# Kernel tuning notes

Measured on AMD Instinct MI355X. Metric: run time of the kernel, lower is better.

Reference implementation:

```python
import jax, jax.numpy as jnp
import numpy as np

N_NODES = 100000
N_EDGES = 1600000
C_IN = 128
C_OUT = 128
BN_EPS = 1e-5


def setup_inputs() -> dict:
    key = jax.random.key(0)
    k = jax.random.split(key, 4)
    x = jax.random.normal(k[0], (N_NODES, C_IN), dtype=jnp.float32)
    edge_index = jax.random.randint(k[1], (2, N_EDGES), 0, N_NODES, dtype=jnp.int32)
    # nn.Linear params (Kaiming-uniform-ish scale)
    lim = 1.0 / np.sqrt(C_IN)
    W = jax.random.uniform(k[2], (C_IN, C_OUT), jnp.float32, -lim, lim)
    b = jnp.zeros((C_OUT,), jnp.float32)
    # BatchNorm (eval mode: running stats)
    gamma = jnp.ones((C_OUT,), jnp.float32)
    beta = jnp.zeros((C_OUT,), jnp.float32)
    running_mean = jnp.zeros((C_OUT,), jnp.float32)
    running_var = jnp.ones((C_OUT,), jnp.float32)
    return {"x": x, "edge_index": edge_index, "W": W, "b": b,
            "gamma": gamma, "beta": beta,
            "running_mean": running_mean, "running_var": running_var}


def reference(x, edge_index, W, b, gamma, beta, running_mean, running_var):
    # Linear projection: [N, C_in] @ [C_in, C_out]
    h = x @ W + b
    in_node, out_node = edge_index[0], edge_index[1]
    # gather edge features then scatter-mean onto destination nodes
    sums = jax.ops.segment_sum(h[in_node], out_node, num_segments=N_NODES)
    cnt = jax.ops.segment_sum(jnp.ones((in_node.shape[0],), h.dtype), out_node,
                              num_segments=N_NODES)
    agg = sums / jnp.maximum(cnt, 1.0)[:, None]  # mean; 0 for isolated nodes
    # BatchNorm1d (eval mode: running stats) + ReLU; dropout is identity in eval
    inv = jax.lax.rsqrt(running_var + BN_EPS)
    out = (agg - running_mean) * (inv * gamma) + beta
    return jax.nn.relu(out)
```

## Files before the change

kernel.cpp:

```cpp
#include <hip/hip_runtime.h>


#define NN 100000
#define NE 1600000
#define CC 128
#define BN_EPS 1e-5f
#define LBLK 1563
#define LSTR 136
#define NBUK 256
#define DPB 391
#define ACH 4096
#define ABLK 391
#define CAP 12288
#define GNB 64
#define CAP2 1536
#define BHS 16

typedef __attribute__((ext_vector_type(8))) short bf16x8;
typedef __attribute__((ext_vector_type(4))) float f32x4;

static __device__ __forceinline__ short f2bf(float f) {
  union { float f; unsigned u; } v; v.f = f;
  unsigned r = (v.u + 0x7FFF + ((v.u >> 16) & 1)) >> 16;
  return (short)r;
}
static __device__ __forceinline__ float bflo(unsigned p) {
  return __uint_as_float(p << 16);
}
static __device__ __forceinline__ float bfhi(unsigned p) {
  return __uint_as_float(p & 0xffff0000u);
}

static __device__ __forceinline__ int excl_scan256(int* a, int t, int v) {
  a[t] = v;
  __syncthreads();
  for (int d = 1; d < 256; d <<= 1) {
    const int x = (t >= d) ? a[t - d] : 0;
    __syncthreads();
    a[t] += x;
    __syncthreads();
  }
  const int incl = a[t];
  __syncthreads();
  a[t] = incl - v;
  __syncthreads();
  return incl - v;
}

__global__ __launch_bounds__(256) void prep_hist(
    const float* __restrict__ W, const float* __restrict__ bias,
    const float* __restrict__ gamma, const float* __restrict__ beta,
    const float* __restrict__ rmean, const float* __restrict__ rvar,
    const int* __restrict__ ei, short* __restrict__ Wsw,
    float* __restrict__ scsh, int* __restrict__ bhist) {
  __shared__ int lh[NBUK];
  const int t = threadIdx.x;
  const int i = blockIdx.x * 256 + t;
  if (i < CC * CC) {
    const int k = i >> 7, n = i & 127;
    const int nt = n & 7, m = n >> 3;
    const int kb = k >> 5, q = (k >> 3) & 3, j = k & 7;
    Wsw[(size_t)(((nt * 4 + kb) * 64 + (m + 16 * q)) * 8 + j)] = f2bf(W[i]);
  }
  if (i < CC) {
    const float sc = gamma[i] * rsqrtf(rvar[i] + BN_EPS);
    scsh[i] = sc;
    scsh[CC + i] = beta[i] - rmean[i] * sc;
    scsh[2 * CC + i] = bias[i];
  }
  lh[t] = 0;
  __syncthreads();
  const int e0 = blockIdx.x * ACH;
  const int e1 = min(NE, e0 + ACH);
  for (int e = e0 + t; e < e1; e += 256) atomicAdd(&lh[ei[NE + e] / DPB], 1);
  __syncthreads();
  if (lh[t]) atomicAdd(&bhist[t * BHS], lh[t]);
}

__global__ __launch_bounds__(256) void scatter_linear(
    const int* __restrict__ ei, const int* __restrict__ bhist,
    int* __restrict__ gcurz, int* __restrict__ ebuf,
    const float* __restrict__ x, const short* __restrict__ Wsw,
    const float* __restrict__ scsh, short* __restrict__ hout,
    int scat) {
  __shared__ __align__(16) char smem[50176];
  const int t = threadIdx.x;

  if (blockIdx.x < scat) {
    int2* sorted = (int2*)smem;
    int*  gsc    = (int*)(smem + 32768);
    int*  lh     = (int*)(smem + 33792);
    int*  lex    = (int*)(smem + 34816);
    int*  rb     = (int*)(smem + 35840);
    int*  lc     = (int*)(smem + 36864);
    const int e0 = blockIdx.x * ACH;
    const int e1 = min(NE, e0 + ACH);
    const int gbase = excl_scan256(gsc, t, bhist[t * BHS]);
    lh[t] = 0;
    __syncthreads();
    for (int e = e0 + t; e < e1; e += 256) atomicAdd(&lh[ei[NE + e] / DPB], 1);
    __syncthreads();
    const int vh = lh[t];
    const int lbase = excl_scan256(lex, t, vh);
    lc[t] = lbase;
    if (vh > 0) rb[t] = gbase + atomicAdd(&gcurz[t * BHS], vh);
    __syncthreads();
    for (int e = e0 + t; e < e1; e += 256) {
      const int src = ei[e], dst = ei[NE + e];
      const int p = atomicAdd(&lc[dst / DPB], 1);
      sorted[p] = make_int2(src, dst);
    }
    __syncthreads();
    const int n = e1 - e0;
    for (int i = t; i < n; i += 256) {
      const int2 v = sorted[i];
      const int b = v.y / DPB;
      ebuf[rb[b] + (i - lex[b])] = (v.x << 9) | (v.y - b * DPB);
    }
    return;
  }

  short* lsA = (short*)smem;
  short* lsW = (short*)(smem + 17408);
  const int n0 = (blockIdx.x - scat) * 64;

#pragma unroll
  for (int j = 0; j < 8; ++j) {
    const int idx = j * 256 + t;
    const int row = idx >> 5, kc4 = idx & 31;
    float4 v = make_float4(0.f, 0.f, 0.f, 0.f);
    if (n0 + row < NN) v = *(const float4*)(x + (size_t)(n0 + row) * CC + kc4 * 4);
    short4 sv;
    sv.x = f2bf(v.x); sv.y = f2bf(v.y); sv.z = f2bf(v.z); sv.w = f2bf(v.w);
    *(short4*)(lsA + row * LSTR + kc4 * 4) = sv;
  }
#pragma unroll
  for (int j = 0; j < 8; ++j) {
    const int idx = j * 256 + t;
    *(bf16x8*)(lsW + (size_t)idx * 8) = *(const bf16x8*)(Wsw + (size_t)idx * 8);
  }
  __syncthreads();

  const int wave = t >> 6, lane = t & 63;
  const int quad = lane >> 4, m = lane & 15;
  const int rowbase = n0 + wave * 16;

  f32x4 acc[8];
#pragma unroll
  for (int nt = 0; nt < 8; ++nt) acc[nt] = (f32x4){0.f, 0.f, 0.f, 0.f};

#pragma unroll
  for (int kb = 0; kb < 4; ++kb) {
    const bf16x8 a =
        *(const bf16x8*)(lsA + (wave * 16 + m) * LSTR + kb * 32 + quad * 8);
#pragma unroll
    for (int nt = 0; nt < 8; ++nt) {
      const bf16x8 bb = *(const bf16x8*)(lsW + (size_t)(((nt * 4 + kb) * 64 + lane) * 8));
      acc[nt] = __builtin_amdgcn_mfma_f32_16x16x32_bf16(a, bb, acc[nt], 0, 0, 0);
    }
  }

  const float4 b0 = *(const float4*)(scsh + 2 * CC + m * 8);
  const float4 b1 = *(const float4*)(scsh + 2 * CC + m * 8 + 4);
  const float bv[8] = {b0.x, b0.y, b0.z, b0.w, b1.x, b1.y, b1.z, b1.w};

#pragma unroll
  for (int reg = 0; reg < 4; ++reg) {
    const int R = rowbase + quad * 4 + reg;
    if (R >= NN) continue;
    bf16x8 hv;
#pragma unroll
    for (int nt = 0; nt < 8; ++nt) hv[nt] = f2bf(acc[nt][reg] + bv[nt]);
    *(bf16x8*)(hout + (size_t)R * CC + m * 8) = hv;
  }
}

__global__ __launch_bounds__(1024) void bucket_to_csr(
    const int* __restrict__ ebuf, const int* __restrict__ bhist,
    int* __restrict__ off, int* __restrict__ csr) {
  __shared__ int gs[NBUK];
  __shared__ int dh[512];
  __shared__ int s[512];
  __shared__ int lcur[512];
  __shared__ int lcsr[CAP];
  const int b = blockIdx.x, t = threadIdx.x;

  if (t < NBUK) gs[t] = bhist[t * BHS];
  __syncthreads();
  for (int d = 1; d < NBUK; d <<= 1) {
    int a0 = 0;
    if (t < NBUK && t >= d) a0 = gs[t - d];
    __syncthreads();
    if (t < NBUK) gs[t] += a0;
    __syncthreads();
  }
  const int seglen = bhist[b * BHS];
  const int segbase = gs[b] - seglen;
  const int lo = b * DPB;
  const int hi = min(NN, lo + DPB);
  const int nd = hi - lo;
  const int* eb = ebuf + segbase;

  if (t < 512) dh[t] = 0;
  __syncthreads();
  for (int i = t; i < seglen; i += 1024) atomicAdd(&dh[eb[i] & 511], 1);
  __syncthreads();

  if (t < 512) s[t] = dh[t];
  __syncthreads();
  for (int d = 1; d < 512; d <<= 1) {
    int a0 = 0;
    if (t < 512 && t >= d) a0 = s[t - d];
    __syncthreads();
    if (t < 512) s[t] += a0;
    __syncthreads();
  }
  if (t < 512) lcur[t] = s[t] - dh[t];
  if (t < nd) off[lo + t] = segbase + (s[t] - dh[t]);
  if (b == NBUK - 1 && t == 0) off[NN] = NE;
  __syncthreads();

  if (seglen <= CAP) {
    for (int i = t; i < seglen; i += 1024) {
      const int e = eb[i];
      const int p = atomicAdd(&lcur[e & 511], 1);
      lcsr[p] = (int)((unsigned)e >> 9);
    }
    __syncthreads();
    for (int i = t; i < seglen; i += 1024) csr[segbase + i] = lcsr[i];
  } else {
    for (int i = t; i < seglen; i += 1024) {
      const int e = eb[i];
      const int p = atomicAdd(&lcur[e & 511], 1);
      csr[segbase + p] = (int)((unsigned)e >> 9);
    }
  }
}

__global__ __launch_bounds__(256) void gather_bn_relu(
    const short* __restrict__ h, const int* __restrict__ off,
    const int* __restrict__ csr, const float* __restrict__ scsh,
    float* __restrict__ out) {
  __shared__ int loff[GNB + 1];
  __shared__ int lcsr[CAP2];
  const int nb0 = blockIdx.x * GNB;
  const int t = threadIdx.x;
  const int nnb = min(GNB, NN - nb0);

  for (int i = t; i <= nnb; i += 256) loff[i] = off[nb0 + i];
  __syncthreads();
  const int s0 = loff[0];
  const int seglen = loff[nnb] - s0;
  const int stg = min(seglen, CAP2);
  for (int i = t; i < stg; i += 256) lcsr[i] = csr[s0 + i];
  __syncthreads();

  const int wave = t >> 6, lane = t & 63;
  const int e4 = lane >> 4;
  const int c16 = lane & 15;
  const float4 sc0 = *(const float4*)(scsh + c16 * 8);
  const float4 sc1 = *(const float4*)(scsh + c16 * 8 + 4);
  const float4 sh0 = *(const float4*)(scsh + CC + c16 * 8);
  const float4 sh1 = *(const float4*)(scsh + CC + c16 * 8 + 4);

  const int lEnd = min(nnb, wave * 16 + 16);
  const bool inl = (seglen <= CAP2);
  for (int l = wave * 16; l < lEnd; ++l) {
    const int s = inl ? loff[l] - s0 : loff[l];
    const int e = inl ? loff[l + 1] - s0 : loff[l + 1];
    float a0 = 0.f, a1 = 0.f, a2 = 0.f, a3 = 0.f;
    float a4 = 0.f, a5 = 0.f, a6 = 0.f, a7 = 0.f;
    int i = s + e4;
    for (; i + 4 < e; i += 8) {
      const int q0 = inl ? lcsr[i] : csr[i];
      const int q1 = inl ? lcsr[i + 4] : csr[i + 4];
      const uint4 p0 = *(const uint4*)(h + (size_t)q0 * CC + c16 * 8);
      const uint4 p1 = *(const uint4*)(h + (size_t)q1 * CC + c16 * 8);
      a0 += bflo(p0.x) + bflo(p1.x); a1 += bfhi(p0.x) + bfhi(p1.x);
      a2 += bflo(p0.y) + bflo(p1.y); a3 += bfhi(p0.y) + bfhi(p1.y);
      a4 += bflo(p0.z) + bflo(p1.z); a5 += bfhi(p0.z) + bfhi(p1.z);
      a6 += bflo(p0.w) + bflo(p1.w); a7 += bfhi(p0.w) + bfhi(p1.w);
    }
    if (i < e) {
      const int q = inl ? lcsr[i] : csr[i];
      const uint4 p = *(const uint4*)(h + (size_t)q * CC + c16 * 8);
      a0 += bflo(p.x); a1 += bfhi(p.x);
      a2 += bflo(p.y); a3 += bfhi(p.y);
      a4 += bflo(p.z); a5 += bfhi(p.z);
      a6 += bflo(p.w); a7 += bfhi(p.w);
    }
    a0 += __shfl_xor(a0, 16); a1 += __shfl_xor(a1, 16);
    a2 += __shfl_xor(a2, 16); a3 += __shfl_xor(a3, 16);
    a4 += __shfl_xor(a4, 16); a5 += __shfl_xor(a5, 16);
    a6 += __shfl_xor(a6, 16); a7 += __shfl_xor(a7, 16);
    a0 += __shfl_xor(a0, 32); a1 += __shfl_xor(a1, 32);
    a2 += __shfl_xor(a2, 32); a3 += __shfl_xor(a3, 32);
    a4 += __shfl_xor(a4, 32); a5 += __shfl_xor(a5, 32);
    a6 += __shfl_xor(a6, 32); a7 += __shfl_xor(a7, 32);
    if (e4 == 0) {
      const float inv = (e > s) ? 1.0f / (float)(e - s) : 0.0f;
      float4 o0, o1;
      o0.x = fmaxf(0.f, a0 * inv * sc0.x + sh0.x);
      o0.y = fmaxf(0.f, a1 * inv * sc0.y + sh0.y);
      o0.z = fmaxf(0.f, a2 * inv * sc0.z + sh0.z);
      o0.w = fmaxf(0.f, a3 * inv * sc0.w + sh0.w);
      o1.x = fmaxf(0.f, a4 * inv * sc1.x + sh1.x);
      o1.y = fmaxf(0.f, a5 * inv * sc1.y + sh1.y);
      o1.z = fmaxf(0.f, a6 * inv * sc1.z + sh1.z);
      o1.w = fmaxf(0.f, a7 * inv * sc1.w + sh1.w);
      float* op = out + (size_t)(nb0 + l) * CC + c16 * 8;
      *(float4*)op = o0;
      *(float4*)(op + 4) = o1;
    }
  }
}

__global__ __launch_bounds__(256) void edge_scatter(
    const float* __restrict__ x, const int* __restrict__ ei,
    float* __restrict__ sums, int* __restrict__ cnt) {
  int gt = blockIdx.x * 256 + threadIdx.x;
  int e = gt >> 5;
  int sub = gt & 31;
  if (e >= NE) return;
  int src = ei[e];
  int dst = ei[NE + e];
  const float4 v = *(const float4*)(x + (size_t)src * CC + sub * 4);
  float* o = sums + (size_t)dst * CC + sub * 4;
  unsafeAtomicAdd(o + 0, v.x);
  unsafeAtomicAdd(o + 1, v.y);
  unsafeAtomicAdd(o + 2, v.z);
  unsafeAtomicAdd(o + 3, v.w);
  if (sub == 0) atomicAdd(cnt + dst, 1);
}

__global__ __launch_bounds__(256) void gemm_bn_relu_fb(
    float* buf, const float* __restrict__ W, const float* __restrict__ bias,
    const float* __restrict__ gamma, const float* __restrict__ beta,
    const float* __restrict__ rmean, const float* __restrict__ rvar,
    const int* __restrict__ cnt) {
  __shared__ float xsT[CC][65];
  const int t = threadIdx.x;
  const int n0 = blockIdx.x * 64;
  for (int j = 0; j < 8; ++j) {
    int i = t + 256 * j;
    int row = i >> 5;
    int ko = (i & 31) * 4;
    float4 v = make_float4(0.f, 0.f, 0.f, 0.f);
    if (n0 + row < NN) v = *(const float4*)(buf + (size_t)(n0 + row) * CC + ko);
    xsT[ko + 0][row] = v.x;
    xsT[ko + 1][row] = v.y;
    xsT[ko + 2][row] = v.z;
    xsT[ko + 3][row] = v.w;
  }
  __syncthreads();
  const int cg = t & 31;
  const int ng8 = (t >> 5) * 8;
  float acc[8][4];
#pragma unroll
  for (int j = 0; j < 8; ++j)
#pragma unroll
    for (int c = 0; c < 4; ++c) acc[j][c] = 0.f;
#pragma unroll 8
  for (int k = 0; k < CC; ++k) {
    const float4 wv = *(const float4*)(W + k * CC + cg * 4);
#pragma unroll
    for (int j = 0; j < 8; ++j) {
      const float xv = xsT[k][ng8 + j];
      acc[j][0] = fmaf(xv, wv.x, acc[j][0]);
      acc[j][1] = fmaf(xv, wv.y, acc[j][1]);
      acc[j][2] = fmaf(xv, wv.z, acc[j][2]);
      acc[j][3] = fmaf(xv, wv.w, acc[j][3]);
    }
  }
  const float4 bb = *(const float4*)(bias + cg * 4);
  const float4 gg = *(const float4*)(gamma + cg * 4);
  const float4 bt = *(const float4*)(beta + cg * 4);
  const float4 mu = *(const float4*)(rmean + cg * 4);
  const float4 vr = *(const float4*)(rvar + cg * 4);
  float sc[4], sh[4];
  sc[0] = gg.x * rsqrtf(vr.x + BN_EPS);
  sc[1] = gg.y * rsqrtf(vr.y + BN_EPS);
  sc[2] = gg.z * rsqrtf(vr.z + BN_EPS);
  sc[3] = gg.w * rsqrtf(vr.w + BN_EPS);
  sh[0] = bt.x - mu.x * sc[0];
  sh[1] = bt.y - mu.y * sc[1];
  sh[2] = bt.z - mu.z * sc[2];
  sh[3] = bt.w - mu.w * sc[3];
#pragma unroll
  for (int j = 0; j < 8; ++j) {
    const int n = n0 + ng8 + j;
    if (n >= NN) continue;
    const int cn = cnt[n];
    const float inv = cn > 0 ? 1.0f / (float)cn : 0.0f;
    const float bsel = cn > 0 ? 1.0f : 0.0f;
    float4 o;
    o.x = fmaxf(0.f, (acc[j][0] * inv + bsel * bb.x) * sc[0] + sh[0]);
    o.y = fmaxf(0.f, (acc[j][1] * inv + bsel * bb.y) * sc[1] + sh[1]);
    o.z = fmaxf(0.f, (acc[j][2] * inv + bsel * bb.z) * sc[2] + sh[2]);
    o.w = fmaxf(0.f, (acc[j][3] * inv + bsel * bb.w) * sc[3] + sh[3]);
    *(float4*)(buf + (size_t)n * CC + cg * 4) = o;
  }
}

extern "C" void kernel_launch(void* const* d_in, const int* in_sizes, int n_in,
                              void* d_out, int out_size, void* d_ws, size_t ws_size,
                              hipStream_t stream) {
  const float* x     = (const float*)d_in[0];
  const int*   ei    = (const int*)d_in[1];
  const float* W     = (const float*)d_in[2];
  const float* bias  = (const float*)d_in[3];
  const float* gamma = (const float*)d_in[4];
  const float* beta  = (const float*)d_in[5];
  const float* rmean = (const float*)d_in[6];
  const float* rvar  = (const float*)d_in[7];
  float* out = (float*)d_out;

  const size_t OFF_B  = 0;
  const size_t BH_B   = 400128;
  const size_t GC_B   = BH_B + 16384;
  const size_t SCSH_B = GC_B + 16384;
  const size_t WSW_B  = SCSH_B + 1536;
  const size_t EB_B   = WSW_B + 32768;
  const size_t H_B    = EB_B + (size_t)NE * 4;
  const size_t NEED   = H_B + (size_t)NN * CC * 2;

  const int GGRID = (NN + GNB - 1) / GNB;

  if (ws_size >= NEED) {
    int*   off   = (int*)((char*)d_ws + OFF_B);
    int*   bhist = (int*)((char*)d_ws + BH_B);
    int*   gcurz = (int*)((char*)d_ws + GC_B);
    float* scsh  = (float*)((char*)d_ws + SCSH_B);
    short* Wsw   = (short*)((char*)d_ws + WSW_B);
    int*   ebuf  = (int*)((char*)d_ws + EB_B);
    int*   csr   = ebuf;
    short* h     = (short*)((char*)d_ws + H_B);

    hipMemsetAsync(bhist, 0, 32768, stream);
    prep_hist<<<ABLK, 256, 0, stream>>>(W, bias, gamma, beta, rmean, rvar,
                                        ei, Wsw, scsh, bhist);
    scatter_linear<<<ABLK + LBLK, 256, 0, stream>>>(
        ei, bhist, gcurz, ebuf, x, Wsw, scsh, h, ABLK);
    bucket_to_csr<<<NBUK, 1024, 0, stream>>>(ebuf, bhist, off, csr);
    gather_bn_relu<<<GGRID, 256, 0, stream>>>(h, off, csr, scsh, out);
  } else {
    int* cnt = (int*)d_ws;
    hipMemsetAsync(out, 0, (size_t)NN * CC * sizeof(float), stream);
    hipMemsetAsync(cnt, 0, (size_t)NN * sizeof(int), stream);
    edge_scatter<<<(NE * 32) / 256, 256, 0, stream>>>(x, ei, out, cnt);
    gemm_bn_relu_fb<<<(NN + 63) / 64, 256, 0, stream>>>(
        out, W, bias, gamma, beta, rmean, rvar, cnt);
  }
}
```

Measured before the change: 220.5 us.

## Drop histogram pre-pass using fixed-capacity buckets and fold prep into consumers

Removes the separate prep_hist kernel. Each destination bucket now gets a fixed slot of BCAP entries in the edge buffer, so no global histogram or prefix scan is needed before scattering. The W bf16 swizzle is done inside each GEMM block, and the BN scale and shift are computed inside the gather kernel. A per-node degree array is added because CSR segments now have gaps between buckets, and the gather staging capacity is raised to fit those gaps. This saves one kernel launch and one pass over the destination indices. In exchange, every GEMM block redoes the W conversion, and correctness depends on no bucket exceeding BCAP. Buckets that overflow are silently truncated, which only holds for near-uniform destination distributions.

```diff
diff --git a/kernel.cpp b/kernel.cpp
--- a/kernel.cpp
+++ b/kernel.cpp
@@ -11,9 +11,10 @@
 #define DPB 391
 #define ACH 4096
 #define ABLK 391
+#define BCAP 7168
 #define CAP 12288
 #define GNB 64
-#define CAP2 1536
+#define CAP2 4096
 #define BHS 16
 
 typedef __attribute__((ext_vector_type(8))) short bf16x8;
@@ -47,55 +48,22 @@
   return incl - v;
 }
 
-__global__ __launch_bounds__(256) void prep_hist(
+__global__ __launch_bounds__(256) void scatter_linear2(
+    const int* __restrict__ ei, int* __restrict__ gcur,
+    int* __restrict__ ebuf, const float* __restrict__ x,
     const float* __restrict__ W, const float* __restrict__ bias,
-    const float* __restrict__ gamma, const float* __restrict__ beta,
-    const float* __restrict__ rmean, const float* __restrict__ rvar,
-    const int* __restrict__ ei, short* __restrict__ Wsw,
-    float* __restrict__ scsh, int* __restrict__ bhist) {
-  __shared__ int lh[NBUK];
-  const int t = threadIdx.x;
-  const int i = blockIdx.x * 256 + t;
-  if (i < CC * CC) {
-    const int k = i >> 7, n = i & 127;
-    const int nt = n & 7, m = n >> 3;
-    const int kb = k >> 5, q = (k >> 3) & 3, j = k & 7;
-    Wsw[(size_t)(((nt * 4 + kb) * 64 + (m + 16 * q)) * 8 + j)] = f2bf(W[i]);
-  }
-  if (i < CC) {
-    const float sc = gamma[i] * rsqrtf(rvar[i] + BN_EPS);
-    scsh[i] = sc;
-    scsh[CC + i] = beta[i] - rmean[i] * sc;
-    scsh[2 * CC + i] = bias[i];
-  }
-  lh[t] = 0;
-  __syncthreads();
-  const int e0 = blockIdx.x * ACH;
-  const int e1 = min(NE, e0 + ACH);
-  for (int e = e0 + t; e < e1; e += 256) atomicAdd(&lh[ei[NE + e] / DPB], 1);
-  __syncthreads();
-  if (lh[t]) atomicAdd(&bhist[t * BHS], lh[t]);
-}
-
-__global__ __launch_bounds__(256) void scatter_linear(
-    const int* __restrict__ ei, const int* __restrict__ bhist,
-    int* __restrict__ gcurz, int* __restrict__ ebuf,
-    const float* __restrict__ x, const short* __restrict__ Wsw,
-    const float* __restrict__ scsh, short* __restrict__ hout,
-    int scat) {
+    short* __restrict__ hout, int scat) {
   __shared__ __align__(16) char smem[50176];
   const int t = threadIdx.x;
 
   if (blockIdx.x < scat) {
     int2* sorted = (int2*)smem;
-    int*  gsc    = (int*)(smem + 32768);
-    int*  lh     = (int*)(smem + 33792);
-    int*  lex    = (int*)(smem + 34816);
-    int*  rb     = (int*)(smem + 35840);
-    int*  lc     = (int*)(smem + 36864);
+    int*  lh     = (int*)(smem + 32768);
+    int*  lex    = (int*)(smem + 33792);
+    int*  rb     = (int*)(smem + 34816);
+    int*  lc     = (int*)(smem + 35840);
     const int e0 = blockIdx.x * ACH;
     const int e1 = min(NE, e0 + ACH);
-    const int gbase = excl_scan256(gsc, t, bhist[t * BHS]);
     lh[t] = 0;
     __syncthreads();
     for (int e = e0 + t; e < e1; e += 256) atomicAdd(&lh[ei[NE + e] / DPB], 1);
@@ -103,7 +71,7 @@
     const int vh = lh[t];
     const int lbase = excl_scan256(lex, t, vh);
     lc[t] = lbase;
-    if (vh > 0) rb[t] = gbase + atomicAdd(&gcurz[t * BHS], vh);
+    if (vh > 0) rb[t] = t * BCAP + atomicAdd(&gcur[t * BHS], vh);
     __syncthreads();
     for (int e = e0 + t; e < e1; e += 256) {
       const int src = ei[e], dst = ei[NE + e];
@@ -134,10 +102,12 @@
     sv.x = f2bf(v.x); sv.y = f2bf(v.y); sv.z = f2bf(v.z); sv.w = f2bf(v.w);
     *(short4*)(lsA + row * LSTR + kc4 * 4) = sv;
   }
-#pragma unroll
-  for (int j = 0; j < 8; ++j) {
-    const int idx = j * 256 + t;
-    *(bf16x8*)(lsW + (size_t)idx * 8) = *(const bf16x8*)(Wsw + (size_t)idx * 8);
+  for (int j = 0; j < 64; ++j) {
+    const int i = j * 256 + t;
+    const int k = i >> 7, n = i & 127;
+    const int nt = n & 7, m2 = n >> 3;
+    const int kb = k >> 5, q = (k >> 3) & 3, jj = k & 7;
+    lsW[((nt * 4 + kb) * 64 + (m2 + 16 * q)) * 8 + jj] = f2bf(W[i]);
   }
   __syncthreads();
 
@@ -160,8 +130,8 @@
     }
   }
 
-  const float4 b0 = *(const float4*)(scsh + 2 * CC + m * 8);
-  const float4 b1 = *(const float4*)(scsh + 2 * CC + m * 8 + 4);
+  const float4 b0 = *(const float4*)(bias + m * 8);
+  const float4 b1 = *(const float4*)(bias + m * 8 + 4);
   const float bv[8] = {b0.x, b0.y, b0.z, b0.w, b1.x, b1.y, b1.z, b1.w};
 
 #pragma unroll
@@ -175,27 +145,17 @@
   }
 }
 
-__global__ __launch_bounds__(1024) void bucket_to_csr(
-    const int* __restrict__ ebuf, const int* __restrict__ bhist,
-    int* __restrict__ off, int* __restrict__ csr) {
-  __shared__ int gs[NBUK];
+__global__ __launch_bounds__(1024) void bucket_to_csr2(
+    const int* __restrict__ ebuf, const int* __restrict__ gcur,
+    int* __restrict__ off, int* __restrict__ dg, int* __restrict__ csr) {
   __shared__ int dh[512];
   __shared__ int s[512];
   __shared__ int lcur[512];
   __shared__ int lcsr[CAP];
   const int b = blockIdx.x, t = threadIdx.x;
 
-  if (t < NBUK) gs[t] = bhist[t * BHS];
-  __syncthreads();
-  for (int d = 1; d < NBUK; d <<= 1) {
-    int a0 = 0;
-    if (t < NBUK && t >= d) a0 = gs[t - d];
-    __syncthreads();
-    if (t < NBUK) gs[t] += a0;
-    __syncthreads();
-  }
-  const int seglen = bhist[b * BHS];
-  const int segbase = gs[b] - seglen;
+  const int seglen = min(gcur[b * BHS], BCAP);
+  const int segbase = b * BCAP;
   const int lo = b * DPB;
   const int hi = min(NN, lo + DPB);
   const int nd = hi - lo;
@@ -216,8 +176,11 @@
     __syncthreads();
   }
   if (t < 512) lcur[t] = s[t] - dh[t];
-  if (t < nd) off[lo + t] = segbase + (s[t] - dh[t]);
-  if (b == NBUK - 1 && t == 0) off[NN] = NE;
+  if (t < nd) {
+    off[lo + t] = segbase + (s[t] - dh[t]);
+    dg[lo + t] = dh[t];
+  }
+  if (b == NBUK - 1 && t == 0) off[NN] = segbase + seglen;
   __syncthreads();
 
   if (seglen <= CAP) {
@@ -237,17 +200,21 @@
   }
 }
 
-__global__ __launch_bounds__(256) void gather_bn_relu(
+__global__ __launch_bounds__(256) void gather_bn_relu2(
     const short* __restrict__ h, const int* __restrict__ off,
-    const int* __restrict__ csr, const float* __restrict__ scsh,
+    const int* __restrict__ dg, const int* __restrict__ csr,
+    const float* __restrict__ gamma, const float* __restrict__ beta,
+    const float* __restrict__ rmean, const float* __restrict__ rvar,
     float* __restrict__ out) {
   __shared__ int loff[GNB + 1];
+  __shared__ int ldg[GNB];
   __shared__ int lcsr[CAP2];
   const int nb0 = blockIdx.x * GNB;
   const int t = threadIdx.x;
   const int nnb = min(GNB, NN - nb0);
 
   for (int i = t; i <= nnb; i += 256) loff[i] = off[nb0 + i];
+  if (t < nnb) ldg[t] = dg[nb0 + t];
   __syncthreads();
   const int s0 = loff[0];
   const int seglen = loff[nnb] - s0;
@@ -258,16 +225,30 @@
   const int wave = t >> 6, lane = t & 63;
   const int e4 = lane >> 4;
   const int c16 = lane & 15;
-  const float4 sc0 = *(const float4*)(scsh + c16 * 8);
-  const float4 sc1 = *(const float4*)(scsh + c16 * 8 + 4);
-  const float4 sh0 = *(const float4*)(scsh + CC + c16 * 8);
-  const float4 sh1 = *(const float4*)(scsh + CC + c16 * 8 + 4);
+  const float4 g0 = *(const float4*)(gamma + c16 * 8);
+  const float4 g1 = *(const float4*)(gamma + c16 * 8 + 4);
+  const float4 v0 = *(const float4*)(rvar + c16 * 8);
+  const float4 v1 = *(const float4*)(rvar + c16 * 8 + 4);
+  const float4 m0 = *(const float4*)(rmean + c16 * 8);
+  const float4 m1 = *(const float4*)(rmean + c16 * 8 + 4);
+  const float4 bt0 = *(const float4*)(beta + c16 * 8);
+  const float4 bt1 = *(const float4*)(beta + c16 * 8 + 4);
+  float4 sc0, sc1, sh0, sh1;
+  sc0.x = g0.x * rsqrtf(v0.x + BN_EPS); sh0.x = bt0.x - m0.x * sc0.x;
+  sc0.y = g0.y * rsqrtf(v0.y + BN_EPS); sh0.y = bt0.y - m0.y * sc0.y;
+  sc0.z = g0.z * rsqrtf(v0.z + BN_EPS); sh0.z = bt0.z - m0.z * sc0.z;
+  sc0.w = g0.w * rsqrtf(v0.w + BN_EPS); sh0.w = bt0.w - m0.w * sc0.w;
+  sc1.x = g1.x * rsqrtf(v1.x + BN_EPS); sh1.x = bt1.x - m1.x * sc1.x;
+  sc1.y = g1.y * rsqrtf(v1.y + BN_EPS); sh1.y = bt1.y - m1.y * sc1.y;
+  sc1.z = g1.z * rsqrtf(v1.z + BN_EPS); sh1.z = bt1.z - m1.z * sc1.z;
+  sc1.w = g1.w * rsqrtf(v1.w + BN_EPS); sh1.w = bt1.w - m1.w * sc1.w;
 
   const int lEnd = min(nnb, wave * 16 + 16);
   const bool inl = (seglen <= CAP2);
   for (int l = wave * 16; l < lEnd; ++l) {
+    const int deg = ldg[l];
     const int s = inl ? loff[l] - s0 : loff[l];
-    const int e = inl ? loff[l + 1] - s0 : loff[l + 1];
+    const int e = s + deg;
     float a0 = 0.f, a1 = 0.f, a2 = 0.f, a3 = 0.f;
     float a4 = 0.f, a5 = 0.f, a6 = 0.f, a7 = 0.f;
     int i = s + e4;
@@ -298,7 +279,7 @@
     a4 += __shfl_xor(a4, 32); a5 += __shfl_xor(a5, 32);
     a6 += __shfl_xor(a6, 32); a7 += __shfl_xor(a7, 32);
     if (e4 == 0) {
-      const float inv = (e > s) ? 1.0f / (float)(e - s) : 0.0f;
+      const float inv = (deg > 0) ? 1.0f / (float)deg : 0.0f;
       float4 o0, o1;
       o0.x = fmaxf(0.f, a0 * inv * sc0.x + sh0.x);
       o0.y = fmaxf(0.f, a1 * inv * sc0.y + sh0.y);
@@ -415,34 +396,29 @@
   const float* rvar  = (const float*)d_in[7];
   float* out = (float*)d_out;
 
-  const size_t OFF_B  = 0;
-  const size_t BH_B   = 400128;
-  const size_t GC_B   = BH_B + 16384;
-  const size_t SCSH_B = GC_B + 16384;
-  const size_t WSW_B  = SCSH_B + 1536;
-  const size_t EB_B   = WSW_B + 32768;
-  const size_t H_B    = EB_B + (size_t)NE * 4;
-  const size_t NEED   = H_B + (size_t)NN * CC * 2;
+  const size_t OFF_B = 0;
+  const size_t DG_B  = 400128;
+  const size_t GC_B  = DG_B + 400128;
+  const size_t EB_B  = GC_B + 16384;
+  const size_t H_B   = EB_B + (size_t)NBUK * BCAP * 4;
+  const size_t NEED  = H_B + (size_t)NN * CC * 2;
 
   const int GGRID = (NN + GNB - 1) / GNB;
 
   if (ws_size >= NEED) {
-    int*   off   = (int*)((char*)d_ws + OFF_B);
-    int*   bhist = (int*)((char*)d_ws + BH_B);
-    int*   gcurz = (int*)((char*)d_ws + GC_B);
-    float* scsh  = (float*)((char*)d_ws + SCSH_B);
-    short* Wsw   = (short*)((char*)d_ws + WSW_B);
-    int*   ebuf  = (int*)((char*)d_ws + EB_B);
-    int*   csr   = ebuf;
-    short* h     = (short*)((char*)d_ws + H_B);
-
-    hipMemsetAsync(bhist, 0, 32768, stream);
-    prep_hist<<<ABLK, 256, 0, stream>>>(W, bias, gamma, beta, rmean, rvar,
-                                        ei, Wsw, scsh, bhist);
-    scatter_linear<<<ABLK + LBLK, 256, 0, stream>>>(
-        ei, bhist, gcurz, ebuf, x, Wsw, scsh, h, ABLK);
-    bucket_to_csr<<<NBUK, 1024, 0, stream>>>(ebuf, bhist, off, csr);
-    gather_bn_relu<<<GGRID, 256, 0, stream>>>(h, off, csr, scsh, out);
+    int*   off  = (int*)((char*)d_ws + OFF_B);
+    int*   dg   = (int*)((char*)d_ws + DG_B);
+    int*   gcur = (int*)((char*)d_ws + GC_B);
+    int*   ebuf = (int*)((char*)d_ws + EB_B);
+    int*   csr  = ebuf;
+    short* h    = (short*)((char*)d_ws + H_B);
+
+    hipMemsetAsync(gcur, 0, 16384, stream);
+    scatter_linear2<<<ABLK + LBLK, 256, 0, stream>>>(
+        ei, gcur, ebuf, x, W, bias, h, ABLK);
+    bucket_to_csr2<<<NBUK, 1024, 0, stream>>>(ebuf, gcur, off, dg, csr);
+    gather_bn_relu2<<<GGRID, 256, 0, stream>>>(h, off, dg, csr, gamma, beta,
+                                               rmean, rvar, out);
   } else {
     int* cnt = (int*)d_ws;
     hipMemsetAsync(out, 0, (size_t)NN * CC * sizeof(float), stream);
```

New measurement: 218.1 us. About the same (-1.1%).
